# Kernel optimization log

Measured on AMD Instinct MI355X. Metric: run time of the kernel, lower is better.

The kernel has to match this reference:

```python
import jax, jax.numpy as jnp
import numpy as np

H = 400   # hidden_size
K = 10    # attention mixture components
V = 77    # window/vocab size
O = 121   # output_size


def lstm_layer(x_seq, W_ih, W_hh, b, h0, c0):
    """Full-sequence LSTM (PyTorch gate order i,f,g,o). x_seq: (B,T,D) -> (B,T,H)."""
    pre = jnp.einsum('btd,gd->btg', x_seq, W_ih) + b  # precompute input contribution
    W_hh_T = W_hh.T

    def step(carry, p_t):
        h, c = carry
        g = p_t + h @ W_hh_T
        i, f, gg, o = jnp.split(g, 4, axis=-1)
        c = jax.nn.sigmoid(f) * c + jax.nn.sigmoid(i) * jnp.tanh(gg)
        h = jax.nn.sigmoid(o) * jnp.tanh(c)
        return (h, c), h

    _, hs = jax.lax.scan(step, (h0, c0), pre.transpose(1, 0, 2))
    return hs.transpose(1, 0, 2)


def setup_inputs():
    key = jax.random.key(0)
    ks = jax.random.split(key, 12)
    B, T, U = 64, 600, 64
    d1, d23 = 3 + V, 3 + V + H
    s = 0.05  # ~sqrt(1/H), matching torch LSTM init scale
    p = lambda k, sh, sc=s: jax.random.normal(k, sh, jnp.float32) * sc
    return dict(
        inputs=jax.random.normal(ks[0], (B, T, 3), jnp.float32),
        text=jax.random.randint(ks[1], (B, U), 0, V),
        text_mask=jnp.ones((B, U), jnp.float32),
        W_ih1=p(ks[2], (4 * H, d1)), W_hh1=p(ks[3], (4 * H, H)), b1=jnp.zeros((4 * H,), jnp.float32),
        W_ih2=p(ks[4], (4 * H, d23)), W_hh2=p(ks[5], (4 * H, H)), b2=jnp.zeros((4 * H,), jnp.float32),
        W_ih3=p(ks[6], (4 * H, d23)), W_hh3=p(ks[7], (4 * H, H)), b3=jnp.zeros((4 * H,), jnp.float32),
        W_win=p(ks[8], (3 * K, H), 0.01), b_win=jnp.zeros((3 * K,), jnp.float32),
        W_out=p(ks[9], (O, 3 * H), 0.1), b_out=jnp.zeros((O,), jnp.float32),
    )


def reference(inputs, text, text_mask, W_ih1, W_hh1, b1, W_ih2, W_hh2, b2,
              W_ih3, W_hh3, b3, W_win, b_win, W_out, b_out):
    B, T, _ = inputs.shape
    U = text.shape[1]
    enc = jax.nn.one_hot(text, V, dtype=inputs.dtype)        # (B,U,V)
    u = jnp.arange(U, dtype=inputs.dtype)                    # char positions
    W_ih1_T, W_hh1_T = W_ih1.T, W_hh1.T

    def step1(carry, x_t):
        h, c, w, kap = carry
        inp = jnp.concatenate([x_t, w], axis=-1)             # (B, 3+V)
        g = inp @ W_ih1_T + h @ W_hh1_T + b1
        i, f, gg, o = jnp.split(g, 4, axis=-1)
        c = jax.nn.sigmoid(f) * c + jax.nn.sigmoid(i) * jnp.tanh(gg)
        h = jax.nn.sigmoid(o) * jnp.tanh(c)
        # Gaussian-mixture attention window
        mix = jnp.exp(h @ W_win.T + b_win)                   # (B, 3K)
        alpha, beta, kappa = jnp.split(mix, 3, axis=-1)      # each (B,K)
        kap = kap + kappa
        phi = jnp.sum(alpha[:, :, None] * jnp.exp(-beta[:, :, None] * (kap[:, :, None] - u) ** 2), axis=1)  # (B,U)
        phi = phi * text_mask
        w = jnp.einsum('bu,buv->bv', phi, enc)               # (B,V)
        return (h, c, w, kap), (h, w)

    zH = jnp.zeros((B, H), inputs.dtype)
    init = (zH, zH, jnp.zeros((B, V), inputs.dtype), jnp.zeros((B, K), inputs.dtype))
    _, (h1s, ws) = jax.lax.scan(step1, init, inputs.transpose(1, 0, 2))
    hid1 = h1s.transpose(1, 0, 2)                            # (B,T,H)
    wvec = ws.transpose(1, 0, 2)                             # (B,T,V)

    hid2 = lstm_layer(jnp.concatenate([inputs, hid1, wvec], axis=-1), W_ih2, W_hh2, b2, zH, zH)
    hid3 = lstm_layer(jnp.concatenate([inputs, hid2, wvec], axis=-1), W_ih3, W_hh3, b3, zH, zH)
    y_hat = jnp.concatenate([hid1, hid2, hid3], axis=-1) @ W_out.T + b_out  # (B,T,O)
    return y_hat
```

## Files before the change

### kernel.cpp

```cpp
#include <hip/hip_runtime.h>
#include <hip/hip_cooperative_groups.h>

namespace cg = cooperative_groups;

#define HH 400
#define NK 10
#define VV 77
#define NO 121
#define TT 600
#define UU 64

#define NWG 256
#define NTH 1024

#define KS  5
#define J1  12
#define J23 22
#define JO  30

#define O_L1  0
#define O_L2  384000
#define O_L3  1088000
#define O_OUT 1792000
#define O_WW  1868800
#define O_XC  1874800

typedef _Float16 h2 __attribute__((ext_vector_type(2)));

struct Args {
  const float* __restrict__ x;
  const int*   __restrict__ text;
  const float* __restrict__ mask;
  const float* __restrict__ Wih1; const float* __restrict__ Whh1; const float* __restrict__ b1;
  const float* __restrict__ Wih2; const float* __restrict__ Whh2; const float* __restrict__ b2;
  const float* __restrict__ Wih3; const float* __restrict__ Whh3; const float* __restrict__ b3;
  const float* __restrict__ Wwin; const float* __restrict__ bwin;
  const float* __restrict__ Wout; const float* __restrict__ bout;
  float* __restrict__ out;
  float* __restrict__ ws;
};

__device__ __forceinline__ float sigm(float v) { return 1.0f / (1.0f + __expf(-v)); }

#if defined(__has_builtin)
#if __has_builtin(__builtin_amdgcn_fdot2)
#define FDOT2(a,b,c) __builtin_amdgcn_fdot2((a),(b),(c),false)
#endif
#endif
#ifndef FDOT2
#define FDOT2(a,b,c) fmaf((float)(a).x,(float)(b).x, fmaf((float)(a).y,(float)(b).y,(c)))
#endif

__device__ __forceinline__ h2 toh2(unsigned int u) { return __builtin_bit_cast(h2, u); }

__device__ __forceinline__ float dot4(uint4 p, uint4 v, float a) {
  a = FDOT2(toh2(p.x), toh2(v.x), a);
  a = FDOT2(toh2(p.y), toh2(v.y), a);
  a = FDOT2(toh2(p.z), toh2(v.z), a);
  a = FDOT2(toh2(p.w), toh2(v.w), a);
  return a;
}

__device__ __forceinline__ unsigned int packh2(float f0, float f1) {
  unsigned short lo = __builtin_bit_cast(unsigned short, (_Float16)f0);
  unsigned short hi = __builtin_bit_cast(unsigned short, (_Float16)f1);
  return (unsigned int)lo | ((unsigned int)hi << 16);
}

__global__ __launch_bounds__(1024) void hsnet_kernel(Args A) {
  cg::grid_group grid = cg::this_grid();
  const int lid  = threadIdx.x;
  const int bid  = blockIdx.x;
  const int band = bid & 7;
  const int grp  = bid >> 3;
  const int lane = lid & 63;
  const int wv   = lid >> 6;
  unsigned int* __restrict__ wsu = (unsigned int*)A.ws;

  for (int i = bid * NTH + lid; i < O_XC; i += NWG * NTH) {
    float f0, f1;
    if (i < O_OUT) {
      const float *Wih, *Whh; int J, LD, rel;
      if (i < O_L2)      { rel = i;          J = J1;  LD = 80;  Wih = A.Wih1; Whh = A.Whh1; }
      else if (i < O_L3) { rel = i - O_L2;   J = J23; LD = 480; Wih = A.Wih2; Whh = A.Whh2; }
      else               { rel = i - O_L3;   J = J23; LD = 480; Wih = A.Wih3; Whh = A.Whh3; }
      int U = rel >> 2, c4 = rel & 3;
      int r = U % 200, T = U / 200;
      int j = T % J,  T2 = T / J;
      int s = T2 % KS, b = T2 / KS;
      int cell = b * 50 + (r % 50), gate = r / 50;
      int grow = gate * 400 + cell;
      int kk = (s * J + j) * 8 + 2 * c4;
      if (kk < LD) { f0 = Wih[grow * LD + kk];        f1 = Wih[grow * LD + kk + 1]; }
      else         { f0 = Whh[grow * 400 + kk - LD];  f1 = Whh[grow * 400 + kk - LD + 1]; }
    } else if (i < O_WW) {
      int rel = i - O_OUT;
      int U = rel >> 2, c4 = rel & 3;
      int o16 = U % 16, T = U / 16;
      int j = T % JO, T2 = T / JO;
      int s = T2 % KS, b = T2 / KS;
      int oglob = 8 * o16 + b;
      int kk = (s * JO + j) * 8 + 2 * c4;
      f0 = (oglob < NO) ? A.Wout[oglob * 1200 + kk]     : 0.f;
      f1 = (oglob < NO) ? A.Wout[oglob * 1200 + kk + 1] : 0.f;
    } else {
      int u = i - O_WW, ln = u / 100, p = u - ln * 100;
      int gw = ln >> 1, half = ln & 1, k0 = half * 200 + 2 * p;
      f0 = A.Wwin[gw * HH + k0]; f1 = A.Wwin[gw * HH + k0 + 1];
    }
    wsu[i] = packh2(f0, f1);
  }
  {
    unsigned long long* xz = (unsigned long long*)(wsu + O_XC);
    for (int i = bid * NTH + lid; i < 32 * 1200; i += NWG * NTH)
      __hip_atomic_store(&xz[i], 0ull, __ATOMIC_RELAXED, __HIP_MEMORY_SCOPE_AGENT);
  }
  grid.sync();

  const uint4* W1b = (const uint4*)(wsu + O_L1)  + (size_t)band * KS * J1  * 200;
  const uint4* W2b = (const uint4*)(wsu + O_L2)  + (size_t)band * KS * J23 * 200;
  const uint4* W3b = (const uint4*)(wsu + O_L3)  + (size_t)band * KS * J23 * 200;
  const uint4* WOb = (const uint4*)(wsu + O_OUT) + (size_t)band * KS * JO  * 16;
  const unsigned int* __restrict__ WWIN = wsu + O_WW;
  unsigned long long* xg = (unsigned long long*)(wsu + O_XC) + (size_t)grp * 1200;

  __shared__ alignas(16) _Float16 svh1[2][480];
  __shared__ alignas(16) _Float16 svh2[2][880];
  __shared__ alignas(16) _Float16 svh3[2][880];
  __shared__ alignas(16) _Float16 soh[2][1200];
  __shared__ float pp[2000];
  __shared__ float pO[160];

  for (int i = lid; i < 960;  i += NTH) (&svh1[0][0])[i] = (_Float16)0.f;
  for (int i = lid; i < 1760; i += NTH) { (&svh2[0][0])[i] = (_Float16)0.f;
                                          (&svh3[0][0])[i] = (_Float16)0.f; }
  for (int i = lid; i < 2400; i += NTH) (&soh[0][0])[i] = (_Float16)0.f;
  if (lid >= 512 && lid < 518) {
    int il = (lid - 512) / 3, cm = (lid - 512) % 3;
    svh1[il][cm] = (_Float16)A.x[(size_t)(2 * grp + il) * TT * 3 + cm];
  }

  const int rg = lid % 200;
  const int sg = lid / 200;
  const int itm = 2 * grp + ((wv < 2) ? wv : 0);
  float maskr = A.mask[itm * UU + lane];
  int   textr = A.text[itm * UU + lane];
  float bwinr = (lane < 60 && !(lane & 1)) ? A.bwin[lane >> 1] : 0.f;
  float kapr[NK];
  #pragma unroll
  for (int k = 0; k < NK; ++k) kapr[k] = 0.f;
  float2 c1 = {0.f, 0.f}, c2r = {0.f, 0.f}, c3r = {0.f, 0.f};
  __syncthreads();

#define GATES(WB, J, V0, V1)                                                  \
    if (sg < KS) {                                                            \
      const uint4* Wp = (WB) + (size_t)(sg * (J)) * 200 + rg;                 \
      const uint4* p0 = (const uint4*)((V0) + sg * (J) * 8);                  \
      const uint4* p1 = (const uint4*)((V1) + sg * (J) * 8);                  \
      float a0 = 0.f, a1 = 0.f;                                               \
      _Pragma("unroll 2")                                                     \
      for (int j = 0; j < (J); ++j) {                                         \
        uint4 w = Wp[(size_t)j * 200];                                        \
        a0 = dot4(w, p0[j], a0); a1 = dot4(w, p1[j], a1);                     \
      }                                                                       \
      pp[(sg * 2 + 0) * 200 + rg] = a0;                                       \
      pp[(sg * 2 + 1) * 200 + rg] = a1;                                       \
    }

#define CELL(B, CREG, PH, GEN, STORES)                                        \
    if (lid < 50) {                                                           \
      int il = lid / 25, pr = lid % 25;                                       \
      float2 hp;                                                              \
      _Pragma("unroll")                                                       \
      for (int e = 0; e < 2; ++e) {                                           \
        int cl = 2 * pr + e;                                                  \
        float gI = 0.f, gF = 0.f, gG = 0.f, gO = 0.f;                         \
        _Pragma("unroll")                                                     \
        for (int s = 0; s < KS; ++s) {                                        \
          const float* b0 = &pp[(s * 2 + il) * 200];                          \
          gI += b0[cl]; gF += b0[50 + cl]; gG += b0[100 + cl]; gO += b0[150 + cl]; \
        }                                                                     \
        int gcell = band * 50 + cl;                                           \
        gI += B[gcell]; gF += B[400 + gcell]; gG += B[800 + gcell]; gO += B[1200 + gcell]; \
        float cc = sigm(gF) * (e ? CREG.y : CREG.x) + sigm(gI) * tanhf(gG);   \
        if (e) CREG.y = cc; else CREG.x = cc;                                 \
        float h = sigm(gO) * tanhf(cc);                                       \
        if (e) hp.y = h; else hp.x = h;                                       \
      }                                                                       \
      h2 hh = { (_Float16)hp.x, (_Float16)hp.y };                             \
      int idx = band * 50 + 2 * pr;                                           \
      unsigned long long tw = ((unsigned long long)(GEN) << 32)               \
                            | (unsigned long long)__builtin_bit_cast(unsigned int, hh); \
      __hip_atomic_store(&xg[(((PH) * 8 + band) * 2 + il) * 25 + pr], tw,     \
                         __ATOMIC_RELAXED, __HIP_MEMORY_SCOPE_AGENT);         \
      STORES                                                                  \
    }

#define POLL(PH, GEN, DESTS)                                                  \
    if (lid < 350) {                                                          \
      int p = lid / 50, w = lid % 50, il = w / 25, pr = w % 25;               \
      int pb = p + (p >= band);                                               \
      const unsigned int gexp = (GEN);                                        \
      unsigned long long v64;                                                 \
      while ((unsigned int)((v64 = __hip_atomic_load(                         \
                 &xg[(((PH) * 8 + pb) * 2 + il) * 25 + pr],                   \
                 __ATOMIC_RELAXED, __HIP_MEMORY_SCOPE_AGENT)) >> 32) != gexp) \
        __builtin_amdgcn_s_sleep(1);                                          \
      h2 hv = toh2((unsigned int)v64);                                        \
      int idx = pb * 50 + 2 * pr;                                             \
      DESTS                                                                   \
    }

  for (int t = 0; t < TT; ++t) {
    if (t > 0 && lid < 32) {
      int oi = lid & 15, il = lid >> 4;
      int o = 8 * oi + band;
      if (o < NO) {
        float r = A.bout[o];
        #pragma unroll
        for (int s = 0; s < KS; ++s) r += pO[(s * 2 + il) * 16 + oi];
        A.out[((size_t)(2 * grp + il) * TT + (t - 1)) * NO + o] = r;
      }
    }
    GATES(W1b, J1, svh1[0], svh1[1])
    __syncthreads();
    CELL(A.b1, c1, 0, 3u * t + 1u,
      soh[il][idx] = hh.x;      soh[il][idx + 1] = hh.y;
      svh1[il][80 + idx] = hh.x; svh1[il][81 + idx] = hh.y;
      svh2[il][3 + idx]  = hh.x; svh2[il][4 + idx]  = hh.y;
    )
    if (lid >= 512 && lid < 518) {
      int il = (lid - 512) / 3, cm = (lid - 512) % 3;
      _Float16 xv = (_Float16)A.x[((size_t)(2 * grp + il) * TT + t) * 3 + cm];
      svh2[il][cm] = xv; svh3[il][cm] = xv;
    }
    POLL(0, 3u * t + 1u,
      soh[il][idx] = hv.x;      soh[il][idx + 1] = hv.y;
      svh1[il][80 + idx] = hv.x; svh1[il][81 + idx] = hv.y;
      svh2[il][3 + idx]  = hv.x; svh2[il][4 + idx]  = hv.y;
    )
    __syncthreads();
    if (wv < 2) {
      const int il = wv;
      const h2* hO = (const h2*)soh[il];
      float m = 0.f;
      if (lane < 60) {
        const uint4* ww = (const uint4*)WWIN + lane * 25;
        const h2* hp = hO + (lane & 1) * 100;
        float acc = 0.f;
        #pragma unroll 5
        for (int p = 0; p < 25; ++p) {
          uint4 wq = ww[p];
          acc = FDOT2(toh2(wq.x), hp[4 * p + 0], acc);
          acc = FDOT2(toh2(wq.y), hp[4 * p + 1], acc);
          acc = FDOT2(toh2(wq.z), hp[4 * p + 2], acc);
          acc = FDOT2(toh2(wq.w), hp[4 * p + 3], acc);
        }
        m = acc;
      }
      m += __shfl_xor(m, 1);
      float mix = 0.f;
      if (lane < 60 && !(lane & 1)) mix = __expf(m + bwinr);
      float alpha[NK], beta[NK];
      #pragma unroll
      for (int k = 0; k < NK; ++k) {
        alpha[k] = __shfl(mix, 2 * k);
        beta[k]  = __shfl(mix, 20 + 2 * k);
        kapr[k] += __shfl(mix, 40 + 2 * k);
      }
      float u = (float)lane, phi = 0.f;
      #pragma unroll
      for (int k = 0; k < NK; ++k) {
        float d = kapr[k] - u;
        phi += alpha[k] * __expf(-beta[k] * d * d);
      }
      phi *= maskr;
      float w0a = 0.f, w1a = 0.f;
      #pragma unroll 8
      for (int uu2 = 0; uu2 < UU; ++uu2) {
        int   tu = __shfl(textr, uu2);
        float pu = __shfl(phi, uu2);
        w0a += (tu == lane)      ? pu : 0.f;
        w1a += (tu == lane + 64) ? pu : 0.f;
      }
      if (lane < VV) {
        _Float16 wh = (_Float16)w0a;
        svh1[il][3 + lane] = wh; svh2[il][403 + lane] = wh; svh3[il][403 + lane] = wh;
      }
      if (lane + 64 < VV) {
        _Float16 wh = (_Float16)w1a;
        svh1[il][67 + lane] = wh; svh2[il][467 + lane] = wh; svh3[il][467 + lane] = wh;
      }
    }
    __syncthreads();
    GATES(W2b, J23, svh2[0], svh2[1])
    __syncthreads();
    CELL(A.b2, c2r, 1, 3u * t + 2u,
      soh[il][400 + idx] = hh.x;  soh[il][401 + idx] = hh.y;
      svh2[il][480 + idx] = hh.x; svh2[il][481 + idx] = hh.y;
      svh3[il][3 + idx]   = hh.x; svh3[il][4 + idx]   = hh.y;
    )
    POLL(1, 3u * t + 2u,
      soh[il][400 + idx] = hv.x;  soh[il][401 + idx] = hv.y;
      svh2[il][480 + idx] = hv.x; svh2[il][481 + idx] = hv.y;
      svh3[il][3 + idx]   = hv.x; svh3[il][4 + idx]   = hv.y;
    )
    __syncthreads();
    GATES(W3b, J23, svh3[0], svh3[1])
    __syncthreads();
    CELL(A.b3, c3r, 2, 3u * t + 3u,
      soh[il][800 + idx] = hh.x;  soh[il][801 + idx] = hh.y;
      svh3[il][480 + idx] = hh.x; svh3[il][481 + idx] = hh.y;
    )
    if (lid >= 512 && lid < 518 && t + 1 < TT) {
      int il = (lid - 512) / 3, cm = (lid - 512) % 3;
      svh1[il][cm] = (_Float16)A.x[((size_t)(2 * grp + il) * TT + (t + 1)) * 3 + cm];
    }
    if (lid >= 64 && lid < 112) {
      int oi = (lid - 64) & 15, s = (lid - 64) >> 4;
      const uint4* Wp = WOb + (size_t)(s * JO) * 16 + oi;
      const uint4* p0 = (const uint4*)(&soh[0][s * 240]);
      const uint4* p1 = (const uint4*)(&soh[1][s * 240]);
      float a0 = 0.f, a1 = 0.f;
      #pragma unroll 3
      for (int j = 0; j < JO; ++j) {
        uint4 w = Wp[(size_t)j * 16];
        a0 = dot4(w, p0[j], a0); a1 = dot4(w, p1[j], a1);
      }
      pO[(s * 2 + 0) * 16 + oi] = a0;
      pO[(s * 2 + 1) * 16 + oi] = a1;
    }
    POLL(2, 3u * t + 3u,
      soh[il][800 + idx] = hv.x;  soh[il][801 + idx] = hv.y;
      svh3[il][480 + idx] = hv.x; svh3[il][481 + idx] = hv.y;
    )
    __syncthreads();
    if (lid < 32) {
      int oi = lid & 15, s = 3 + (lid >> 4);
      const uint4* Wp = WOb + (size_t)(s * JO) * 16 + oi;
      const uint4* p0 = (const uint4*)(&soh[0][s * 240]);
      const uint4* p1 = (const uint4*)(&soh[1][s * 240]);
      float a0 = 0.f, a1 = 0.f;
      #pragma unroll 3
      for (int j = 0; j < JO; ++j) {
        uint4 w = Wp[(size_t)j * 16];
        a0 = dot4(w, p0[j], a0); a1 = dot4(w, p1[j], a1);
      }
      pO[(s * 2 + 0) * 16 + oi] = a0;
      pO[(s * 2 + 1) * 16 + oi] = a1;
    }
    __syncthreads();
  }
  if (lid < 32) {
    int oi = lid & 15, il = lid >> 4;
    int o = 8 * oi + band;
    if (o < NO) {
      float r = A.bout[o];
      #pragma unroll
      for (int s = 0; s < KS; ++s) r += pO[(s * 2 + il) * 16 + oi];
      A.out[((size_t)(2 * grp + il) * TT + (TT - 1)) * NO + o] = r;
    }
  }
#undef GATES
#undef CELL
#undef POLL
}

extern "C" void kernel_launch(void* const* d_in, const int* in_sizes, int n_in,
                              void* d_out, int out_size, void* d_ws, size_t ws_size,
                              hipStream_t stream) {
  Args a;
  a.x    = (const float*)d_in[0];
  a.text = (const int*)  d_in[1];
  a.mask = (const float*)d_in[2];
  a.Wih1 = (const float*)d_in[3];  a.Whh1 = (const float*)d_in[4];  a.b1 = (const float*)d_in[5];
  a.Wih2 = (const float*)d_in[6];  a.Whh2 = (const float*)d_in[7];  a.b2 = (const float*)d_in[8];
  a.Wih3 = (const float*)d_in[9];  a.Whh3 = (const float*)d_in[10]; a.b3 = (const float*)d_in[11];
  a.Wwin = (const float*)d_in[12]; a.bwin = (const float*)d_in[13];
  a.Wout = (const float*)d_in[14]; a.bout = (const float*)d_in[15];
  a.out  = (float*)d_out;
  a.ws   = (float*)d_ws;
  void* kargs[] = { &a };
  hipLaunchCooperativeKernel((const void*)hsnet_kernel, dim3(NWG), dim3(NTH),
                             kargs, 0, stream);
}
```

Before: 16.48 ms.

## Overlap non-recurrent gate partials with polling and split output projection

Splits the layer 2/3 gate matvec into a 12-chunk part that depends on the freshly computed recurrent inputs and a 50-chunk part over inputs already available (previous hidden state and window). The latter is computed by otherwise idle threads during the wait for other workgroups, into separate shared buffers ppB/ppC. Polling moves to the top 128 threads, and the output projection is spread across three phases with register accumulation. This is meant to shorten the critical path per timestep. It costs more shared memory and relies on correct index bookkeeping for the data each partial reads.

New measurement: 19.90 ms. +20.7%, slower.

```diff
diff --git a/kernel.cpp b/kernel.cpp
--- a/kernel.cpp
+++ b/kernel.cpp
@@ -129,6 +129,8 @@
   __shared__ alignas(16) _Float16 svh3[2][880];
   __shared__ alignas(16) _Float16 soh[2][1200];
   __shared__ float pp[2000];
+  __shared__ float ppB[1600];
+  __shared__ float ppC[1600];
   __shared__ float pO[160];
 
   for (int i = lid; i < 960;  i += NTH) (&svh1[0][0])[i] = (_Float16)0.f;
@@ -152,14 +154,14 @@
   float2 c1 = {0.f, 0.f}, c2r = {0.f, 0.f}, c3r = {0.f, 0.f};
   __syncthreads();
 
-#define GATES(WB, J, V0, V1)                                                  \
+#define GATES12(WB, V0, V1)                                                   \
     if (sg < KS) {                                                            \
-      const uint4* Wp = (WB) + (size_t)(sg * (J)) * 200 + rg;                 \
-      const uint4* p0 = (const uint4*)((V0) + sg * (J) * 8);                  \
-      const uint4* p1 = (const uint4*)((V1) + sg * (J) * 8);                  \
+      const uint4* Wp = (WB) + (size_t)(sg * 12) * 200 + rg;                  \
+      const uint4* p0 = (const uint4*)(V0) + sg * 12;                         \
+      const uint4* p1 = (const uint4*)(V1) + sg * 12;                         \
       float a0 = 0.f, a1 = 0.f;                                               \
       _Pragma("unroll 2")                                                     \
-      for (int j = 0; j < (J); ++j) {                                         \
+      for (int j = 0; j < 12; ++j) {                                          \
         uint4 w = Wp[(size_t)j * 200];                                        \
         a0 = dot4(w, p0[j], a0); a1 = dot4(w, p1[j], a1);                     \
       }                                                                       \
@@ -167,7 +169,26 @@
       pp[(sg * 2 + 1) * 200 + rg] = a1;                                       \
     }
 
-#define CELL(B, CREG, PH, GEN, STORES)                                        \
+#define GATESB(WB, V0, V1, PPB, LB)                                           \
+    if (lid >= (LB) && lid < (LB) + 800) {                                    \
+      int t2 = lid - (LB);                                                    \
+      int rgb = t2 % 200, bs = t2 / 200;                                      \
+      int g0 = 60 + bs * 13 - ((bs >= 2) ? (bs - 2) : 0);                     \
+      int cnt = (bs < 2) ? 13 : 12;                                           \
+      const uint4* Wp = (WB) + (size_t)g0 * 200 + rgb;                        \
+      const uint4* p0 = (const uint4*)(V0) + g0;                              \
+      const uint4* p1 = (const uint4*)(V1) + g0;                              \
+      float a0 = 0.f, a1 = 0.f;                                               \
+      _Pragma("unroll 2")                                                     \
+      for (int j = 0; j < cnt; ++j) {                                         \
+        uint4 w = Wp[(size_t)j * 200];                                        \
+        a0 = dot4(w, p0[j], a0); a1 = dot4(w, p1[j], a1);                     \
+      }                                                                       \
+      (PPB)[(bs * 2 + 0) * 200 + rgb] = a0;                                   \
+      (PPB)[(bs * 2 + 1) * 200 + rgb] = a1;                                   \
+    }
+
+#define CELL(B, CREG, PH, GEN, PPX, NB, STORES)                               \
     if (lid < 50) {                                                           \
       int il = lid / 25, pr = lid % 25;                                       \
       float2 hp;                                                              \
@@ -178,6 +199,11 @@
         _Pragma("unroll")                                                     \
         for (int s = 0; s < KS; ++s) {                                        \
           const float* b0 = &pp[(s * 2 + il) * 200];                          \
+          gI += b0[cl]; gF += b0[50 + cl]; gG += b0[100 + cl]; gO += b0[150 + cl]; \
+        }                                                                     \
+        _Pragma("unroll")                                                     \
+        for (int s = 0; s < (NB); ++s) {                                      \
+          const float* b0 = &(PPX)[(s * 2 + il) * 200];                       \
           gI += b0[cl]; gF += b0[50 + cl]; gG += b0[100 + cl]; gO += b0[150 + cl]; \
         }                                                                     \
         int gcell = band * 50 + cl;                                           \
@@ -197,21 +223,41 @@
     }
 
 #define POLL(PH, GEN, DESTS)                                                  \
-    if (lid < 350) {                                                          \
-      int p = lid / 50, w = lid % 50, il = w / 25, pr = w % 25;               \
-      int pb = p + (p >= band);                                               \
+    if (lid >= 896) {                                                         \
       const unsigned int gexp = (GEN);                                        \
-      unsigned long long v64;                                                 \
-      while ((unsigned int)((v64 = __hip_atomic_load(                         \
-                 &xg[(((PH) * 8 + pb) * 2 + il) * 25 + pr],                   \
-                 __ATOMIC_RELAXED, __HIP_MEMORY_SCOPE_AGENT)) >> 32) != gexp) \
-        __builtin_amdgcn_s_sleep(1);                                          \
-      h2 hv = toh2((unsigned int)v64);                                        \
-      int idx = pb * 50 + 2 * pr;                                             \
-      DESTS                                                                   \
+      _Pragma("unroll")                                                       \
+      for (int rep = 0; rep < 3; ++rep) {                                     \
+        int task = (lid - 896) + rep * 128;                                   \
+        if (task < 350) {                                                     \
+          int p = task / 50, w2 = task % 50, il = w2 / 25, pr = w2 % 25;      \
+          int pb = p + (p >= band);                                           \
+          unsigned long long v64;                                             \
+          while ((unsigned int)((v64 = __hip_atomic_load(                     \
+                     &xg[(((PH) * 8 + pb) * 2 + il) * 25 + pr],               \
+                     __ATOMIC_RELAXED, __HIP_MEMORY_SCOPE_AGENT)) >> 32) != gexp) \
+            __builtin_amdgcn_s_sleep(1);                                      \
+          h2 hv = toh2((unsigned int)v64);                                    \
+          int idx = pb * 50 + 2 * pr;                                         \
+          DESTS                                                               \
+        }                                                                     \
+      }                                                                       \
+    }
+
+#define OUTP(BASE)                                                            \
+    if (lid >= 64 && lid < 144) {                                             \
+      int oi = (lid - 64) & 15, sgo = (lid - 64) >> 4;                        \
+      const uint4* Wp = WOb + (size_t)((BASE) + sgo * 10) * 16 + oi;          \
+      const uint4* p0 = (const uint4*)soh[0] + ((BASE) + sgo * 10);           \
+      const uint4* p1 = (const uint4*)soh[1] + ((BASE) + sgo * 10);           \
+      _Pragma("unroll 2")                                                     \
+      for (int j = 0; j < 10; ++j) {                                          \
+        uint4 w = Wp[(size_t)j * 16];                                         \
+        oa0 = dot4(w, p0[j], oa0); oa1 = dot4(w, p1[j], oa1);                 \
+      }                                                                       \
     }
 
   for (int t = 0; t < TT; ++t) {
+    float oa0 = 0.f, oa1 = 0.f;
     if (t > 0 && lid < 32) {
       int oi = lid & 15, il = lid >> 4;
       int o = 8 * oi + band;
@@ -222,18 +268,19 @@
         A.out[((size_t)(2 * grp + il) * TT + (t - 1)) * NO + o] = r;
       }
     }
-    GATES(W1b, J1, svh1[0], svh1[1])
-    __syncthreads();
-    CELL(A.b1, c1, 0, 3u * t + 1u,
+    GATES12(W1b, svh1[0], svh1[1])
+    __syncthreads();
+    CELL(A.b1, c1, 0, 3u * t + 1u, pp, 0,
       soh[il][idx] = hh.x;      soh[il][idx + 1] = hh.y;
       svh1[il][80 + idx] = hh.x; svh1[il][81 + idx] = hh.y;
       svh2[il][3 + idx]  = hh.x; svh2[il][4 + idx]  = hh.y;
     )
-    if (lid >= 512 && lid < 518) {
-      int il = (lid - 512) / 3, cm = (lid - 512) % 3;
+    if (lid >= 50 && lid < 56) {
+      int il = (lid - 50) / 3, cm = (lid - 50) % 3;
       _Float16 xv = (_Float16)A.x[((size_t)(2 * grp + il) * TT + t) * 3 + cm];
       svh2[il][cm] = xv; svh3[il][cm] = xv;
     }
+    GATESB(W2b, svh2[0], svh2[1], ppB, 64)
     POLL(0, 3u * t + 1u,
       soh[il][idx] = hv.x;      soh[il][idx + 1] = hv.y;
       svh1[il][80 + idx] = hv.x; svh1[il][81 + idx] = hv.y;
@@ -292,62 +339,43 @@
         svh1[il][67 + lane] = wh; svh2[il][467 + lane] = wh; svh3[il][467 + lane] = wh;
       }
     }
-    __syncthreads();
-    GATES(W2b, J23, svh2[0], svh2[1])
-    __syncthreads();
-    CELL(A.b2, c2r, 1, 3u * t + 2u,
+    GATESB(W3b, svh3[0], svh3[1], ppC, 128)
+    __syncthreads();
+    GATES12(W2b, svh2[0], svh2[1])
+    __syncthreads();
+    CELL(A.b2, c2r, 1, 3u * t + 2u, ppB, 4,
       soh[il][400 + idx] = hh.x;  soh[il][401 + idx] = hh.y;
       svh2[il][480 + idx] = hh.x; svh2[il][481 + idx] = hh.y;
       svh3[il][3 + idx]   = hh.x; svh3[il][4 + idx]   = hh.y;
     )
+    OUTP(0)
     POLL(1, 3u * t + 2u,
       soh[il][400 + idx] = hv.x;  soh[il][401 + idx] = hv.y;
       svh2[il][480 + idx] = hv.x; svh2[il][481 + idx] = hv.y;
       svh3[il][3 + idx]   = hv.x; svh3[il][4 + idx]   = hv.y;
     )
     __syncthreads();
-    GATES(W3b, J23, svh3[0], svh3[1])
-    __syncthreads();
-    CELL(A.b3, c3r, 2, 3u * t + 3u,
+    GATES12(W3b, svh3[0], svh3[1])
+    __syncthreads();
+    CELL(A.b3, c3r, 2, 3u * t + 3u, ppC, 4,
       soh[il][800 + idx] = hh.x;  soh[il][801 + idx] = hh.y;
       svh3[il][480 + idx] = hh.x; svh3[il][481 + idx] = hh.y;
     )
-    if (lid >= 512 && lid < 518 && t + 1 < TT) {
-      int il = (lid - 512) / 3, cm = (lid - 512) % 3;
+    if (lid >= 50 && lid < 56 && t + 1 < TT) {
+      int il = (lid - 50) / 3, cm = (lid - 50) % 3;
       svh1[il][cm] = (_Float16)A.x[((size_t)(2 * grp + il) * TT + (t + 1)) * 3 + cm];
     }
-    if (lid >= 64 && lid < 112) {
-      int oi = (lid - 64) & 15, s = (lid - 64) >> 4;
-      const uint4* Wp = WOb + (size_t)(s * JO) * 16 + oi;
-      const uint4* p0 = (const uint4*)(&soh[0][s * 240]);
-      const uint4* p1 = (const uint4*)(&soh[1][s * 240]);
-      float a0 = 0.f, a1 = 0.f;
-      #pragma unroll 3
-      for (int j = 0; j < JO; ++j) {
-        uint4 w = Wp[(size_t)j * 16];
-        a0 = dot4(w, p0[j], a0); a1 = dot4(w, p1[j], a1);
-      }
-      pO[(s * 2 + 0) * 16 + oi] = a0;
-      pO[(s * 2 + 1) * 16 + oi] = a1;
-    }
+    OUTP(50)
     POLL(2, 3u * t + 3u,
       soh[il][800 + idx] = hv.x;  soh[il][801 + idx] = hv.y;
       svh3[il][480 + idx] = hv.x; svh3[il][481 + idx] = hv.y;
     )
     __syncthreads();
-    if (lid < 32) {
-      int oi = lid & 15, s = 3 + (lid >> 4);
-      const uint4* Wp = WOb + (size_t)(s * JO) * 16 + oi;
-      const uint4* p0 = (const uint4*)(&soh[0][s * 240]);
-      const uint4* p1 = (const uint4*)(&soh[1][s * 240]);
-      float a0 = 0.f, a1 = 0.f;
-      #pragma unroll 3
-      for (int j = 0; j < JO; ++j) {
-        uint4 w = Wp[(size_t)j * 16];
-        a0 = dot4(w, p0[j], a0); a1 = dot4(w, p1[j], a1);
-      }
-      pO[(s * 2 + 0) * 16 + oi] = a0;
-      pO[(s * 2 + 1) * 16 + oi] = a1;
+    OUTP(100)
+    if (lid >= 64 && lid < 144) {
+      int oi = (lid - 64) & 15, sgo = (lid - 64) >> 4;
+      pO[(sgo * 2 + 0) * 16 + oi] = oa0;
+      pO[(sgo * 2 + 1) * 16 + oi] = oa1;
     }
     __syncthreads();
   }
@@ -361,9 +389,11 @@
       A.out[((size_t)(2 * grp + il) * TT + (TT - 1)) * NO + o] = r;
     }
   }
-#undef GATES
+#undef GATES12
+#undef GATESB
 #undef CELL
 #undef POLL
+#undef OUTP
 }
 
 extern "C" void kernel_launch(void* const* d_in, const int* in_sizes, int n_in,
```

## Assign one batch item per workgroup with 512 blocks of 512 threads

Applied to the files above, without the earlier changes.

Moves from 256 workgroups of 1024 threads, each handling two batch items, to 512 workgroups of 512 threads, each handling one item. The gate dot product is now split over two k-halves instead of five slices, and the poll and cell work shrinks accordingly. The aim is more parallelism and less per-block work on the serial recurrence. In exchange each weight slice is read by twice as many workgroups, and the cross-workgroup flag sync now spans more blocks.

Result: slower. 23.39 ms (+41.9%).

```diff
diff --git a/kernel.cpp b/kernel.cpp
--- a/kernel.cpp
+++ b/kernel.cpp
@@ -10,13 +10,15 @@
 #define TT 600
 #define UU 64
 
-#define NWG 256
-#define NTH 1024
+#define NWG 512
+#define NTH 512
 
 #define KS  5
 #define J1  12
 #define J23 22
 #define JO  30
+#define JH1  30
+#define JH23 55
 
 #define O_L1  0
 #define O_L2  384000
@@ -67,12 +69,12 @@
   return (unsigned int)lo | ((unsigned int)hi << 16);
 }
 
-__global__ __launch_bounds__(1024) void hsnet_kernel(Args A) {
+__global__ __launch_bounds__(512, 8) void hsnet_kernel(Args A) {
   cg::grid_group grid = cg::this_grid();
   const int lid  = threadIdx.x;
   const int bid  = blockIdx.x;
   const int band = bid & 7;
-  const int grp  = bid >> 3;
+  const int item = bid >> 3;
   const int lane = lid & 63;
   const int wv   = lid >> 6;
   unsigned int* __restrict__ wsu = (unsigned int*)A.ws;
@@ -112,7 +114,7 @@
   }
   {
     unsigned long long* xz = (unsigned long long*)(wsu + O_XC);
-    for (int i = bid * NTH + lid; i < 32 * 1200; i += NWG * NTH)
+    for (int i = bid * NTH + lid; i < 64 * 600; i += NWG * NTH)
       __hip_atomic_store(&xz[i], 0ull, __ATOMIC_RELAXED, __HIP_MEMORY_SCOPE_AGENT);
   }
   grid.sync();
@@ -122,29 +124,25 @@
   const uint4* W3b = (const uint4*)(wsu + O_L3)  + (size_t)band * KS * J23 * 200;
   const uint4* WOb = (const uint4*)(wsu + O_OUT) + (size_t)band * KS * JO  * 16;
   const unsigned int* __restrict__ WWIN = wsu + O_WW;
-  unsigned long long* xg = (unsigned long long*)(wsu + O_XC) + (size_t)grp * 1200;
-
-  __shared__ alignas(16) _Float16 svh1[2][480];
-  __shared__ alignas(16) _Float16 svh2[2][880];
-  __shared__ alignas(16) _Float16 svh3[2][880];
-  __shared__ alignas(16) _Float16 soh[2][1200];
-  __shared__ float pp[2000];
-  __shared__ float pO[160];
-
-  for (int i = lid; i < 960;  i += NTH) (&svh1[0][0])[i] = (_Float16)0.f;
-  for (int i = lid; i < 1760; i += NTH) { (&svh2[0][0])[i] = (_Float16)0.f;
-                                          (&svh3[0][0])[i] = (_Float16)0.f; }
-  for (int i = lid; i < 2400; i += NTH) (&soh[0][0])[i] = (_Float16)0.f;
-  if (lid >= 512 && lid < 518) {
-    int il = (lid - 512) / 3, cm = (lid - 512) % 3;
-    svh1[il][cm] = (_Float16)A.x[(size_t)(2 * grp + il) * TT * 3 + cm];
-  }
+  unsigned long long* xg = (unsigned long long*)(wsu + O_XC) + (size_t)item * 600;
+
+  __shared__ alignas(16) _Float16 svh1[480];
+  __shared__ alignas(16) _Float16 svh2[880];
+  __shared__ alignas(16) _Float16 svh3[880];
+  __shared__ alignas(16) _Float16 soh[1200];
+  __shared__ float pp[400];
+  __shared__ float pO[80];
+
+  for (int i = lid; i < 480;  i += NTH) svh1[i] = (_Float16)0.f;
+  for (int i = lid; i < 880;  i += NTH) { svh2[i] = (_Float16)0.f; svh3[i] = (_Float16)0.f; }
+  for (int i = lid; i < 1200; i += NTH) soh[i] = (_Float16)0.f;
+  __syncthreads();
+  if (lid < 3) svh1[lid] = (_Float16)A.x[(size_t)item * TT * 3 + lid];
 
   const int rg = lid % 200;
-  const int sg = lid / 200;
-  const int itm = 2 * grp + ((wv < 2) ? wv : 0);
-  float maskr = A.mask[itm * UU + lane];
-  int   textr = A.text[itm * UU + lane];
+  const int hg = lid / 200;
+  float maskr = A.mask[item * UU + lane];
+  int   textr = A.text[item * UU + lane];
   float bwinr = (lane < 60 && !(lane & 1)) ? A.bwin[lane >> 1] : 0.f;
   float kapr[NK];
   #pragma unroll
@@ -152,34 +150,27 @@
   float2 c1 = {0.f, 0.f}, c2r = {0.f, 0.f}, c3r = {0.f, 0.f};
   __syncthreads();
 
-#define GATES(WB, J, V0, V1)                                                  \
-    if (sg < KS) {                                                            \
-      const uint4* Wp = (WB) + (size_t)(sg * (J)) * 200 + rg;                 \
-      const uint4* p0 = (const uint4*)((V0) + sg * (J) * 8);                  \
-      const uint4* p1 = (const uint4*)((V1) + sg * (J) * 8);                  \
-      float a0 = 0.f, a1 = 0.f;                                               \
+#define GATES(WB, JH)                                                         \
+    if (hg < 2) {                                                             \
+      const uint4* Wp = (WB) + (size_t)(hg * (JH)) * 200 + rg;                \
+      float a0 = 0.f;                                                         \
       _Pragma("unroll 2")                                                     \
-      for (int j = 0; j < (J); ++j) {                                         \
-        uint4 w = Wp[(size_t)j * 200];                                        \
-        a0 = dot4(w, p0[j], a0); a1 = dot4(w, p1[j], a1);                     \
-      }                                                                       \
-      pp[(sg * 2 + 0) * 200 + rg] = a0;                                       \
-      pp[(sg * 2 + 1) * 200 + rg] = a1;                                       \
+      for (int j = 0; j < (JH); ++j)                                          \
+        a0 = dot4(Wp[(size_t)j * 200], vp0[hg * (JH) + j], a0);               \
+      pp[hg * 200 + rg] = a0;                                                 \
     }
 
 #define CELL(B, CREG, PH, GEN, STORES)                                        \
-    if (lid < 50) {                                                           \
-      int il = lid / 25, pr = lid % 25;                                       \
+    if (lid < 25) {                                                           \
+      int pr = lid;                                                           \
       float2 hp;                                                              \
       _Pragma("unroll")                                                       \
       for (int e = 0; e < 2; ++e) {                                           \
         int cl = 2 * pr + e;                                                  \
-        float gI = 0.f, gF = 0.f, gG = 0.f, gO = 0.f;                         \
-        _Pragma("unroll")                                                     \
-        for (int s = 0; s < KS; ++s) {                                        \
-          const float* b0 = &pp[(s * 2 + il) * 200];                          \
-          gI += b0[cl]; gF += b0[50 + cl]; gG += b0[100 + cl]; gO += b0[150 + cl]; \
-        }                                                                     \
+        float gI = pp[cl]       + pp[200 + cl];                               \
+        float gF = pp[50 + cl]  + pp[250 + cl];                               \
+        float gG = pp[100 + cl] + pp[300 + cl];                               \
+        float gO = pp[150 + cl] + pp[350 + cl];                               \
         int gcell = band * 50 + cl;                                           \
         gI += B[gcell]; gF += B[400 + gcell]; gG += B[800 + gcell]; gO += B[1200 + gcell]; \
         float cc = sigm(gF) * (e ? CREG.y : CREG.x) + sigm(gI) * tanhf(gG);   \
@@ -191,19 +182,20 @@
       int idx = band * 50 + 2 * pr;                                           \
       unsigned long long tw = ((unsigned long long)(GEN) << 32)               \
                             | (unsigned long long)__builtin_bit_cast(unsigned int, hh); \
-      __hip_atomic_store(&xg[(((PH) * 8 + band) * 2 + il) * 25 + pr], tw,     \
+      __hip_atomic_store(&xg[((PH) * 8 + band) * 25 + pr], tw,                \
                          __ATOMIC_RELAXED, __HIP_MEMORY_SCOPE_AGENT);         \
       STORES                                                                  \
     }
 
 #define POLL(PH, GEN, DESTS)                                                  \
-    if (lid < 350) {                                                          \
-      int p = lid / 50, w = lid % 50, il = w / 25, pr = w % 25;               \
+    if (lid >= 337) {                                                         \
+      int task = lid - 337;                                                   \
+      int p = task / 25, pr = task % 25;                                      \
       int pb = p + (p >= band);                                               \
       const unsigned int gexp = (GEN);                                        \
       unsigned long long v64;                                                 \
       while ((unsigned int)((v64 = __hip_atomic_load(                         \
-                 &xg[(((PH) * 8 + pb) * 2 + il) * 25 + pr],                   \
+                 &xg[((PH) * 8 + pb) * 25 + pr],                              \
                  __ATOMIC_RELAXED, __HIP_MEMORY_SCOPE_AGENT)) >> 32) != gexp) \
         __builtin_amdgcn_s_sleep(1);                                          \
       h2 hv = toh2((unsigned int)v64);                                        \
@@ -211,38 +203,39 @@
       DESTS                                                                   \
     }
 
+  const uint4* vp0;
+
   for (int t = 0; t < TT; ++t) {
-    if (t > 0 && lid < 32) {
-      int oi = lid & 15, il = lid >> 4;
-      int o = 8 * oi + band;
+    if (t > 0 && lid < 16) {
+      int o = 8 * lid + band;
       if (o < NO) {
         float r = A.bout[o];
         #pragma unroll
-        for (int s = 0; s < KS; ++s) r += pO[(s * 2 + il) * 16 + oi];
-        A.out[((size_t)(2 * grp + il) * TT + (t - 1)) * NO + o] = r;
-      }
-    }
-    GATES(W1b, J1, svh1[0], svh1[1])
+        for (int s = 0; s < KS; ++s) r += pO[s * 16 + lid];
+        A.out[((size_t)item * TT + (t - 1)) * NO + o] = r;
+      }
+    }
+    vp0 = (const uint4*)svh1;
+    GATES(W1b, JH1)
     __syncthreads();
     CELL(A.b1, c1, 0, 3u * t + 1u,
-      soh[il][idx] = hh.x;      soh[il][idx + 1] = hh.y;
-      svh1[il][80 + idx] = hh.x; svh1[il][81 + idx] = hh.y;
-      svh2[il][3 + idx]  = hh.x; svh2[il][4 + idx]  = hh.y;
-    )
-    if (lid >= 512 && lid < 518) {
-      int il = (lid - 512) / 3, cm = (lid - 512) % 3;
-      _Float16 xv = (_Float16)A.x[((size_t)(2 * grp + il) * TT + t) * 3 + cm];
-      svh2[il][cm] = xv; svh3[il][cm] = xv;
+      soh[idx] = hh.x;       soh[idx + 1] = hh.y;
+      svh1[80 + idx] = hh.x; svh1[81 + idx] = hh.y;
+      svh2[3 + idx]  = hh.x; svh2[4 + idx]  = hh.y;
+    )
+    if (lid >= 32 && lid < 35) {
+      int cm = lid - 32;
+      _Float16 xv = (_Float16)A.x[((size_t)item * TT + t) * 3 + cm];
+      svh2[cm] = xv; svh3[cm] = xv;
     }
     POLL(0, 3u * t + 1u,
-      soh[il][idx] = hv.x;      soh[il][idx + 1] = hv.y;
-      svh1[il][80 + idx] = hv.x; svh1[il][81 + idx] = hv.y;
-      svh2[il][3 + idx]  = hv.x; svh2[il][4 + idx]  = hv.y;
-    )
-    __syncthreads();
-    if (wv < 2) {
-      const int il = wv;
-      const h2* hO = (const h2*)soh[il];
+      soh[idx] = hv.x;       soh[idx + 1] = hv.y;
+      svh1[80 + idx] = hv.x; svh1[81 + idx] = hv.y;
+      svh2[3 + idx]  = hv.x; svh2[4 + idx]  = hv.y;
+    )
+    __syncthreads();
+    if (wv == 0) {
+      const h2* hO = (const h2*)soh;
       float m = 0.f;
       if (lane < 60) {
         const uint4* ww = (const uint4*)WWIN + lane * 25;
@@ -285,80 +278,73 @@
       }
       if (lane < VV) {
         _Float16 wh = (_Float16)w0a;
-        svh1[il][3 + lane] = wh; svh2[il][403 + lane] = wh; svh3[il][403 + lane] = wh;
+        svh1[3 + lane] = wh; svh2[403 + lane] = wh; svh3[403 + lane] = wh;
       }
       if (lane + 64 < VV) {
         _Float16 wh = (_Float16)w1a;
-        svh1[il][67 + lane] = wh; svh2[il][467 + lane] = wh; svh3[il][467 + lane] = wh;
-      }
-    }
-    __syncthreads();
-    GATES(W2b, J23, svh2[0], svh2[1])
+        svh1[67 + lane] = wh; svh2[467 + lane] = wh; svh3[467 + lane] = wh;
+      }
+    }
+    __syncthreads();
+    vp0 = (const uint4*)svh2;
+    GATES(W2b, JH23)
     __syncthreads();
     CELL(A.b2, c2r, 1, 3u * t + 2u,
-      soh[il][400 + idx] = hh.x;  soh[il][401 + idx] = hh.y;
-      svh2[il][480 + idx] = hh.x; svh2[il][481 + idx] = hh.y;
-      svh3[il][3 + idx]   = hh.x; svh3[il][4 + idx]   = hh.y;
+      soh[400 + idx] = hh.x;  soh[401 + idx] = hh.y;
+      svh2[480 + idx] = hh.x; svh2[481 + idx] = hh.y;
+      svh3[3 + idx]   = hh.x; svh3[4 + idx]   = hh.y;
     )
     POLL(1, 3u * t + 2u,
-      soh[il][400 + idx] = hv.x;  soh[il][401 + idx] = hv.y;
-      svh2[il][480 + idx] = hv.x; svh2[il][481 + idx] = hv.y;
-      svh3[il][3 + idx]   = hv.x; svh3[il][4 + idx]   = hv.y;
-    )
-    __syncthreads();
-    GATES(W3b, J23, svh3[0], svh3[1])
+      soh[400 + idx] = hv.x;  soh[401 + idx] = hv.y;
+      svh2[480 + idx] = hv.x; svh2[481 + idx] = hv.y;
+      svh3[3 + idx]   = hv.x; svh3[4 + idx]   = hv.y;
+    )
+    __syncthreads();
+    vp0 = (const uint4*)svh3;
+    GATES(W3b, JH23)
     __syncthreads();
     CELL(A.b3, c3r, 2, 3u * t + 3u,
-      soh[il][800 + idx] = hh.x;  soh[il][801 + idx] = hh.y;
-      svh3[il][480 + idx] = hh.x; svh3[il][481 + idx] = hh.y;
-    )
-    if (lid >= 512 && lid < 518 && t + 1 < TT) {
-      int il = (lid - 512) / 3, cm = (lid - 512) % 3;
-      svh1[il][cm] = (_Float16)A.x[((size_t)(2 * grp + il) * TT + (t + 1)) * 3 + cm];
+      soh[800 + idx] = hh.x;  soh[801 + idx] = hh.y;
+      svh3[480 + idx] = hh.x; svh3[481 + idx] = hh.y;
+    )
+    if (lid >= 32 && lid < 35 && t + 1 < TT) {
+      int cm = lid - 32;
+      svh1[cm] = (_Float16)A.x[((size_t)item * TT + (t + 1)) * 3 + cm];
     }
     if (lid >= 64 && lid < 112) {
       int oi = (lid - 64) & 15, s = (lid - 64) >> 4;
       const uint4* Wp = WOb + (size_t)(s * JO) * 16 + oi;
-      const uint4* p0 = (const uint4*)(&soh[0][s * 240]);
-      const uint4* p1 = (const uint4*)(&soh[1][s * 240]);
-      float a0 = 0.f, a1 = 0.f;
+      const uint4* p0 = (const uint4*)soh + s * JO;
+      float a = 0.f;
       #pragma unroll 3
-      for (int j = 0; j < JO; ++j) {
-        uint4 w = Wp[(size_t)j * 16];
-        a0 = dot4(w, p0[j], a0); a1 = dot4(w, p1[j], a1);
-      }
-      pO[(s * 2 + 0) * 16 + oi] = a0;
-      pO[(s * 2 + 1) * 16 + oi] = a1;
+      for (int j = 0; j < JO; ++j)
+        a = dot4(Wp[(size_t)j * 16], p0[j], a);
+      pO[s * 16 + oi] = a;
     }
     POLL(2, 3u * t + 3u,
-      soh[il][800 + idx] = hv.x;  soh[il][801 + idx] = hv.y;
-      svh3[il][480 + idx] = hv.x; svh3[il][481 + idx] = hv.y;
+      soh[800 + idx] = hv.x;  soh[801 + idx] = hv.y;
+      svh3[480 + idx] = hv.x; svh3[481 + idx] = hv.y;
     )
     __syncthreads();
     if (lid < 32) {
       int oi = lid & 15, s = 3 + (lid >> 4);
       const uint4* Wp = WOb + (size_t)(s * JO) * 16 + oi;
-      const uint4* p0 = (const uint4*)(&soh[0][s * 240]);
-      const uint4* p1 = (const uint4*)(&soh[1][s * 240]);
-      float a0 = 0.f, a1 = 0.f;
+      const uint4* p0 = (const uint4*)soh + s * JO;
+      float a = 0.f;
       #pragma unroll 3
-      for (int j = 0; j < JO; ++j) {
-        uint4 w = Wp[(size_t)j * 16];
-        a0 = dot4(w, p0[j], a0); a1 = dot4(w, p1[j], a1);
-      }
-      pO[(s * 2 + 0) * 16 + oi] = a0;
-      pO[(s * 2 + 1) * 16 + oi] = a1;
+      for (int j = 0; j < JO; ++j)
+        a = dot4(Wp[(size_t)j * 16], p0[j], a);
+      pO[s * 16 + oi] = a;
     }
     __syncthreads();
   }
-  if (lid < 32) {
-    int oi = lid & 15, il = lid >> 4;
-    int o = 8 * oi + band;
+  if (lid < 16) {
+    int o = 8 * lid + band;
     if (o < NO) {
       float r = A.bout[o];
       #pragma unroll
-      for (int s = 0; s < KS; ++s) r += pO[(s * 2 + il) * 16 + oi];
-      A.out[((size_t)(2 * grp + il) * TT + (TT - 1)) * NO + o] = r;
+      for (int s = 0; s < KS; ++s) r += pO[s * 16 + lid];
+      A.out[((size_t)item * TT + (TT - 1)) * NO + o] = r;
     }
   }
 #undef GATES
```

## Defer output-projection slices into next timestep to drop a per-step barrier

Applied to the files above, without the earlier changes.

The output projection work for slices 3-4 and the final reduction and store of the previous timestep are moved into the next iteration, overlapping with the layer-1 poll and the attention phase. This removes one __syncthreads and a serialized tail segment per timestep. Poll threads are shifted to lanes 64-413 so they do not collide with the output-projection threads at 448+. The cost is a one-step skew in output writes plus an epilogue after the loop, and it relies on soh slices 3-4 (the layer-2/3 hidden state) not being overwritten before they are consumed.

After: 15.68 ms, median of 2. 4.9% less time.

```diff
diff --git a/kernel.cpp b/kernel.cpp
--- a/kernel.cpp
+++ b/kernel.cpp
@@ -197,8 +197,9 @@
     }
 
 #define POLL(PH, GEN, DESTS)                                                  \
-    if (lid < 350) {                                                          \
-      int p = lid / 50, w = lid % 50, il = w / 25, pr = w % 25;               \
+    if (lid >= 64 && lid < 414) {                                             \
+      int task = lid - 64;                                                    \
+      int p = task / 50, w = task % 50, il = w / 25, pr = w % 25;             \
       int pb = p + (p >= band);                                               \
       const unsigned int gexp = (GEN);                                        \
       unsigned long long v64;                                                 \
@@ -211,17 +212,23 @@
       DESTS                                                                   \
     }
 
+#define OUTS(S0, S1, LB)                                                      \
+    if (lid >= (LB) && lid < (LB) + ((S1) - (S0)) * 16) {                     \
+      int oi = (lid - (LB)) & 15, s = (S0) + ((lid - (LB)) >> 4);             \
+      const uint4* Wp = WOb + (size_t)(s * JO) * 16 + oi;                     \
+      const uint4* p0 = (const uint4*)(&soh[0][s * 240]);                     \
+      const uint4* p1 = (const uint4*)(&soh[1][s * 240]);                     \
+      float a0 = 0.f, a1 = 0.f;                                               \
+      _Pragma("unroll 3")                                                     \
+      for (int j = 0; j < JO; ++j) {                                          \
+        uint4 w = Wp[(size_t)j * 16];                                         \
+        a0 = dot4(w, p0[j], a0); a1 = dot4(w, p1[j], a1);                     \
+      }                                                                       \
+      pO[(s * 2 + 0) * 16 + oi] = a0;                                         \
+      pO[(s * 2 + 1) * 16 + oi] = a1;                                         \
+    }
+
   for (int t = 0; t < TT; ++t) {
-    if (t > 0 && lid < 32) {
-      int oi = lid & 15, il = lid >> 4;
-      int o = 8 * oi + band;
-      if (o < NO) {
-        float r = A.bout[o];
-        #pragma unroll
-        for (int s = 0; s < KS; ++s) r += pO[(s * 2 + il) * 16 + oi];
-        A.out[((size_t)(2 * grp + il) * TT + (t - 1)) * NO + o] = r;
-      }
-    }
     GATES(W1b, J1, svh1[0], svh1[1])
     __syncthreads();
     CELL(A.b1, c1, 0, 3u * t + 1u,
@@ -234,6 +241,7 @@
       _Float16 xv = (_Float16)A.x[((size_t)(2 * grp + il) * TT + t) * 3 + cm];
       svh2[il][cm] = xv; svh3[il][cm] = xv;
     }
+    if (t > 0) { OUTS(3, 5, 448) }
     POLL(0, 3u * t + 1u,
       soh[il][idx] = hv.x;      soh[il][idx + 1] = hv.y;
       svh1[il][80 + idx] = hv.x; svh1[il][81 + idx] = hv.y;
@@ -292,6 +300,16 @@
         svh1[il][67 + lane] = wh; svh2[il][467 + lane] = wh; svh3[il][467 + lane] = wh;
       }
     }
+    if (t > 0 && lid >= 128 && lid < 160) {
+      int k2 = lid - 128, oi = k2 & 15, il = k2 >> 4;
+      int o = 8 * oi + band;
+      if (o < NO) {
+        float r = A.bout[o];
+        #pragma unroll
+        for (int s = 0; s < KS; ++s) r += pO[(s * 2 + il) * 16 + oi];
+        A.out[((size_t)(2 * grp + il) * TT + (t - 1)) * NO + o] = r;
+      }
+    }
     __syncthreads();
     GATES(W2b, J23, svh2[0], svh2[1])
     __syncthreads();
@@ -316,41 +334,15 @@
       int il = (lid - 512) / 3, cm = (lid - 512) % 3;
       svh1[il][cm] = (_Float16)A.x[((size_t)(2 * grp + il) * TT + (t + 1)) * 3 + cm];
     }
-    if (lid >= 64 && lid < 112) {
-      int oi = (lid - 64) & 15, s = (lid - 64) >> 4;
-      const uint4* Wp = WOb + (size_t)(s * JO) * 16 + oi;
-      const uint4* p0 = (const uint4*)(&soh[0][s * 240]);
-      const uint4* p1 = (const uint4*)(&soh[1][s * 240]);
-      float a0 = 0.f, a1 = 0.f;
-      #pragma unroll 3
-      for (int j = 0; j < JO; ++j) {
-        uint4 w = Wp[(size_t)j * 16];
-        a0 = dot4(w, p0[j], a0); a1 = dot4(w, p1[j], a1);
-      }
-      pO[(s * 2 + 0) * 16 + oi] = a0;
-      pO[(s * 2 + 1) * 16 + oi] = a1;
-    }
+    OUTS(0, 3, 448)
     POLL(2, 3u * t + 3u,
       soh[il][800 + idx] = hv.x;  soh[il][801 + idx] = hv.y;
       svh3[il][480 + idx] = hv.x; svh3[il][481 + idx] = hv.y;
     )
     __syncthreads();
-    if (lid < 32) {
-      int oi = lid & 15, s = 3 + (lid >> 4);
-      const uint4* Wp = WOb + (size_t)(s * JO) * 16 + oi;
-      const uint4* p0 = (const uint4*)(&soh[0][s * 240]);
-      const uint4* p1 = (const uint4*)(&soh[1][s * 240]);
-      float a0 = 0.f, a1 = 0.f;
-      #pragma unroll 3
-      for (int j = 0; j < JO; ++j) {
-        uint4 w = Wp[(size_t)j * 16];
-        a0 = dot4(w, p0[j], a0); a1 = dot4(w, p1[j], a1);
-      }
-      pO[(s * 2 + 0) * 16 + oi] = a0;
-      pO[(s * 2 + 1) * 16 + oi] = a1;
-    }
-    __syncthreads();
-  }
+  }
+  OUTS(3, 5, 448)
+  __syncthreads();
   if (lid < 32) {
     int oi = lid & 15, il = lid >> 4;
     int o = 8 * oi + band;
@@ -364,6 +356,7 @@
 #undef GATES
 #undef CELL
 #undef POLL
+#undef OUTS
 }
 
 extern "C" void kernel_launch(void* const* d_in, const int* in_sizes, int n_in,
```
